# Optimization experiments

Measured on AMD Instinct MI355X. Metric: run time of the kernel, lower is better.

The kernel has to match this reference:

```python
import jax, jax.numpy as jnp
import numpy as np
from jax import lax

HEATMAP_THRESH = 0.1


def _conv(x, w, b, stride=1):
    y = lax.conv_general_dilated(x, w, (stride, stride), 'SAME',
                                 dimension_numbers=('NCHW', 'OIHW', 'NCHW'))
    return y + b[None, :, None, None]


def _maxpool2(x):
    return lax.reduce_window(x, -jnp.inf, lax.max, (1, 1, 2, 2), (1, 1, 2, 2), 'VALID')


def _up2(x):
    return jnp.repeat(jnp.repeat(x, 2, axis=2), 2, axis=3)


def _find_peaks_mask(hm, thresh):
    # Vectorized equivalent of the CPU nested-loop _find_peaks:
    # interior pixel is a peak iff v > thresh and v >= its 4 axial neighbors.
    c = hm[:, :, 1:-1, 1:-1]
    m = ((c > thresh)
         & (c >= hm[:, :, :-2, 1:-1]) & (c >= hm[:, :, 2:, 1:-1])
         & (c >= hm[:, :, 1:-1, :-2]) & (c >= hm[:, :, 1:-1, 2:]))
    return jnp.pad(m, ((0, 0), (0, 0), (1, 1), (1, 1)))  # border never a peak


def _param(key, shape):
    fan_in = int(np.prod(shape[1:]))
    return jax.random.normal(key, shape, jnp.float32) / np.sqrt(fan_in)


_SHAPES = {
    'w_d1': (32, 3, 3, 3), 'w_d2': (64, 32, 3, 3), 'w_bn': (128, 64, 3, 3),
    'w_u1': (64, 192, 3, 3), 'w_u2': (32, 96, 3, 3), 'w_seg': (1, 32, 1, 1),
    'w_p1': (64, 4, 3, 3), 'w_p2': (128, 64, 3, 3),
    'w_hm': (17, 128, 1, 1), 'w_paf': (32, 128, 1, 1),
}


def setup_inputs() -> dict:
    key = jax.random.key(0)
    ks = jax.random.split(key, 1 + len(_SHAPES))
    B, H, W = 8, 384, 384
    inp = {'x': jax.random.normal(ks[0], (B, 3, H, W), jnp.float32)}
    for i, (n, s) in enumerate(_SHAPES.items()):
        inp[n] = _param(ks[i + 1], s)
        inp[n.replace('w_', 'b_')] = jnp.zeros((s[0],), jnp.float32)
    return inp


def _forward(x, w_d1, b_d1, w_d2, b_d2, w_bn, b_bn, w_u1, b_u1, w_u2, b_u2,
             w_seg, b_seg, w_p1, b_p1, w_p2, b_p2, w_hm, b_hm, w_paf, b_paf):
    # --- UNet segmentation ---
    d1 = jax.nn.relu(_conv(x, w_d1, b_d1))                    # [B,32,384,384]
    d2 = jax.nn.relu(_conv(_maxpool2(d1), w_d2, b_d2))        # [B,64,192,192]
    bn = jax.nn.relu(_conv(_maxpool2(d2), w_bn, b_bn))        # [B,128,96,96]
    u1 = jax.nn.relu(_conv(jnp.concatenate([_up2(bn), d2], 1), w_u1, b_u1))  # [B,64,192,192]
    u2 = jax.nn.relu(_conv(jnp.concatenate([_up2(u1), d1], 1), w_u2, b_u2))  # [B,32,384,384]
    seg = _conv(u2, w_seg, b_seg)                             # [B,1,384,384]
    # --- Pose net on image + detached seg logits ---
    xp = jnp.concatenate([x, lax.stop_gradient(seg)], axis=1)  # detach()
    p1 = jax.nn.relu(_conv(xp, w_p1, b_p1, stride=2))          # [B,64,192,192]
    p2 = jax.nn.relu(_conv(p1, w_p2, b_p2, stride=2))          # [B,128,96,96]
    hm = _conv(p2, w_hm, b_hm)                                 # [B,17,96,96]
    paf = _conv(p2, w_paf, b_paf)                              # [B,32,96,96]
    return seg, hm, paf


def reference(x, w_d1, b_d1, w_d2, b_d2, w_bn, b_bn, w_u1, b_u1, w_u2, b_u2,
              w_seg, b_seg, w_p1, b_p1, w_p2, b_p2, w_hm, b_hm, w_paf, b_paf):
    seg, hm, paf = _forward(x, w_d1, b_d1, w_d2, b_d2, w_bn, b_bn, w_u1, b_u1,
                            w_u2, b_u2, w_seg, b_seg, w_p1, b_p1, w_p2, b_p2,
                            w_hm, b_hm, w_paf, b_paf)
    # jit-friendly replacement for the variable-length python peak lists:
    # boolean mask over [B,K,h,w]; (x,y) coords recoverable via jnp.nonzero offline.
    peaks = _find_peaks_mask(hm, HEATMAP_THRESH)
    return seg, hm, paf, peaks
```

## Files before the change

kernel.cpp:

```cpp
#include <hip/hip_runtime.h>


#define BS 256
#define BSW 512

typedef _Float16 half8 __attribute__((ext_vector_type(8)));
typedef float floatx4 __attribute__((ext_vector_type(4)));

#define LDSDW 20
#define PLT8 10000
#define ESTR 388

__global__ __launch_bounds__(BS) void packw_gen_kernel(
    const float* __restrict__ w, _Float16* __restrict__ bp, int Cin, int Cout)
{
    int total = (Cin >> 5) * 9 * (Cout >> 4) * 64;
    int tid = blockIdx.x * BS + threadIdx.x;
    if (tid >= total) return;
    int lane = tid & 63;
    int t = tid >> 6;
    int NTl = Cout >> 4;
    int nt = t % NTl; t /= NTl;
    int tap = t % 9;
    int chunk = t / 9;
    int q = lane >> 4, n = lane & 15;
    int co = nt * 16 + n;
    _Float16* ph = bp + (size_t)tid * 8;
    _Float16* pl = bp + (size_t)total * 8 + (size_t)tid * 8;
#pragma unroll
    for (int j = 0; j < 8; ++j) {
        int ci = chunk * 32 + q * 8 + j;
        float v = w[((size_t)co * Cin + ci) * 9 + tap];
        _Float16 h = (_Float16)v;
        ph[j] = h;
        pl[j] = (_Float16)(v - (float)h);
    }
}

__global__ __launch_bounds__(BS) void packw_1x1_kernel(
    const float* __restrict__ w, _Float16* __restrict__ bp, int Cin, int NTl, int Cout)
{
    int total = (Cin >> 5) * NTl * 64;
    int tid = blockIdx.x * BS + threadIdx.x;
    if (tid >= total) return;
    int lane = tid & 63;
    int t = tid >> 6;
    int nt = t % NTl;
    int chunk = t / NTl;
    int q = lane >> 4, n = lane & 15;
    int co = nt * 16 + n;
    _Float16* ph = bp + (size_t)tid * 8;
    _Float16* pl = bp + (size_t)total * 8 + (size_t)tid * 8;
#pragma unroll
    for (int j = 0; j < 8; ++j) {
        int ci = chunk * 32 + q * 8 + j;
        float v = (co < Cout) ? w[(size_t)co * Cin + ci] : 0.f;
        _Float16 h = (_Float16)v;
        ph[j] = h;
        pl[j] = (_Float16)(v - (float)h);
    }
}

template <int CHUNKS, int NT, int HH, int WW, int OUTMODE>
__global__ __launch_bounds__(BS) void conv3x3_mfma_kernel(
    const float* __restrict__ in_,
    const _Float16* __restrict__ bp,
    const float* __restrict__ bias,
    float* __restrict__ out,
    _Float16* __restrict__ osph,
    _Float16* __restrict__ ospl)
{
    constexpr int PL = 4 * 34 * LDSDW;
    constexpr int EPI = 64 * NT * 16;
    constexpr int LDS_DW = (2 * PL > EPI) ? 2 * PL : EPI;
    __shared__ unsigned int lds[LDS_DW];

    int xblks = WW / 32;
    int b = blockIdx.x;
    int xb = b % xblks; b /= xblks;
    int yp = b % (HH / 2);
    int n  = b / (HH / 2);
    int y0 = yp * 2;
    int x0 = xb * 32;

    int tid = threadIdx.x;
    int lane = tid & 63, wv = tid >> 6;
    int m = lane & 15, q = lane >> 4;
    int lrow = wv >> 1;
    int lx   = (wv & 1) * 16;

    floatx4 acc[NT];
#pragma unroll
    for (int nt = 0; nt < NT; ++nt) acc[nt] = (floatx4){0.f, 0.f, 0.f, 0.f};

    const int planeW = CHUNKS * 9 * NT * 64 * 8;

    for (int chunk = 0; chunk < CHUNKS; ++chunk) {
        __syncthreads();
        for (int e = tid; e < 4 * 34 * 4; e += BS) {
            int xi = e % 34;
            int rest = e / 34;
            int oct = rest & 3;
            int row = rest >> 2;
            int iy = y0 - 1 + row, gx = x0 - 1 + xi;
            bool ok = (iy >= 0 && iy < HH && gx >= 0 && gx < WW);
            const float* gp = in_ +
                ((size_t)(n * (CHUNKS * 32) + chunk * 32 + oct * 8) * HH + iy) * WW + gx;
            half8 hv, lv;
#pragma unroll
            for (int j = 0; j < 8; ++j) {
                float v = ok ? gp[(size_t)j * HH * WW] : 0.f;
                _Float16 h = (_Float16)v;
                hv[j] = h;
                lv[j] = (_Float16)(v - (float)h);
            }
            int base = (row * 34 + xi) * LDSDW + oct * 4;
            *(half8*)((char*)lds + (size_t)base * 4) = hv;
            *(half8*)((char*)lds + ((size_t)PL + base) * 4) = lv;
        }
        __syncthreads();
#pragma unroll
        for (int ky = 0; ky < 3; ++ky) {
#pragma unroll
            for (int kx = 0; kx < 3; ++kx) {
                int row = lrow + ky;
                int xi  = lx + m + kx;
                int adw = (row * 34 + xi) * LDSDW + q * 4;
                half8 ah = *(const half8*)((const char*)lds + (size_t)adw * 4);
                half8 al = *(const half8*)((const char*)lds + ((size_t)PL + adw) * 4);
                int tap = ky * 3 + kx;
                const _Float16* bpp = bp + ((size_t)(chunk * 9 + tap) * NT) * 64 * 8;
#pragma unroll
                for (int nt = 0; nt < NT; ++nt) {
                    half8 bh = *(const half8*)(bpp + ((size_t)nt * 64 + lane) * 8);
                    half8 bl = *(const half8*)(bpp + planeW + ((size_t)nt * 64 + lane) * 8);
                    acc[nt] = __builtin_amdgcn_mfma_f32_16x16x32_f16(ah, bh, acc[nt], 0, 0, 0);
                    acc[nt] = __builtin_amdgcn_mfma_f32_16x16x32_f16(ah, bl, acc[nt], 0, 0, 0);
                    acc[nt] = __builtin_amdgcn_mfma_f32_16x16x32_f16(al, bh, acc[nt], 0, 0, 0);
                }
            }
        }
    }

    __syncthreads();
#pragma unroll
    for (int nt = 0; nt < NT; ++nt) {
#pragma unroll
        for (int r = 0; r < 4; ++r) {
            int co = nt * 16 + m;
            int pxl = wv * 16 + q * 4 + r;
            ((float*)lds)[co * 64 + pxl] = acc[nt][r];
        }
    }
    __syncthreads();
    if (OUTMODE != 1) {
        constexpr int thPerCo = 256 / (NT * 16);
        constexpr int pxPerTh = 64 / thPerCo;
        int co = tid / thPerCo;
        int sub = tid % thPerCo;
        int pxb = sub * pxPerTh;
        float bb = bias[co];
#pragma unroll
        for (int u = 0; u < pxPerTh; u += 4) {
            int p = pxb + u;
            int row = y0 + (p >> 5), xx = x0 + (p & 31);
            const float* lp = (const float*)lds + co * 64 + p;
            float4 vv = *(const float4*)lp;
            vv.x = fmaxf(vv.x + bb, 0.f);
            vv.y = fmaxf(vv.y + bb, 0.f);
            vv.z = fmaxf(vv.z + bb, 0.f);
            vv.w = fmaxf(vv.w + bb, 0.f);
            *(float4*)(out + ((size_t)(n * NT * 16 + co) * HH + row) * WW + xx) = vv;
        }
    }
    if (OUTMODE >= 1) {
        constexpr int OCTS = NT * 2;
        for (int it = tid; it < OCTS * 64; it += BS) {
            int px = it & 63;
            int oct = it >> 6;
            int row = y0 + (px >> 5), xx = x0 + (px & 31);
            half8 hv, lv;
#pragma unroll
            for (int j = 0; j < 8; ++j) {
                float v = fmaxf(((float*)lds)[(oct * 8 + j) * 64 + px] + bias[oct * 8 + j], 0.f);
                _Float16 hh = (_Float16)v;
                hv[j] = hh;
                lv[j] = (_Float16)(v - (float)hh);
            }
            size_t oaddr = ((size_t)((n * OCTS + oct) * HH + row) * WW + xx) * 8;
            *(half8*)(osph + oaddr) = hv;
            *(half8*)(ospl + oaddr) = lv;
        }
    }
}

template <int CHUNKS, int NT, int WI>
__global__ __launch_bounds__(BS) void conv3x3s2_mfma_kernel(
    const float* __restrict__ in_,
    const _Float16* __restrict__ bp,
    const float* __restrict__ bias,
    float* __restrict__ out)
{
    constexpr int WO = WI / 2;
    constexpr int PLs = 5 * 68 * LDSDW;
    constexpr int EPI = 64 * NT * 16;
    constexpr int LDS_DW = (2 * PLs > EPI) ? 2 * PLs : EPI;
    __shared__ unsigned int lds[LDS_DW];

    int xblks = WO / 32;
    int b = blockIdx.x;
    int xb = b % xblks; b /= xblks;
    int yp = b % (WO / 2);
    int n  = b / (WO / 2);
    int y0 = yp * 2;
    int x0 = xb * 32;

    int tid = threadIdx.x;
    int lane = tid & 63, wv = tid >> 6;
    int m = lane & 15, q = lane >> 4;
    int lrow = wv >> 1;
    int lx   = (wv & 1) * 16;

    floatx4 acc[NT];
#pragma unroll
    for (int nt = 0; nt < NT; ++nt) acc[nt] = (floatx4){0.f, 0.f, 0.f, 0.f};

    const int planeW = CHUNKS * 9 * NT * 64 * 8;

    for (int chunk = 0; chunk < CHUNKS; ++chunk) {
        __syncthreads();
        for (int e = tid; e < 5 * 68 * 4; e += BS) {
            int xi = e % 68;
            int rest = e / 68;
            int oct = rest & 3;
            int row = rest >> 2;
            int iy = 2 * y0 + row, ix = 2 * x0 + xi;
            bool ok = (xi < 65 && iy < WI && ix < WI);
            const float* gp = in_ +
                ((size_t)(n * (CHUNKS * 32) + chunk * 32 + oct * 8) * WI + iy) * WI + ix;
            half8 hv, lv;
#pragma unroll
            for (int j = 0; j < 8; ++j) {
                float v = ok ? gp[(size_t)j * WI * WI] : 0.f;
                _Float16 h = (_Float16)v;
                hv[j] = h;
                lv[j] = (_Float16)(v - (float)h);
            }
            int pos = (xi & 1) * 34 + (xi >> 1);
            int base = (row * 68 + pos) * LDSDW + oct * 4;
            *(half8*)((char*)lds + (size_t)base * 4) = hv;
            *(half8*)((char*)lds + ((size_t)PLs + base) * 4) = lv;
        }
        __syncthreads();
#pragma unroll
        for (int ky = 0; ky < 3; ++ky) {
#pragma unroll
            for (int kx = 0; kx < 3; ++kx) {
                int row = 2 * lrow + ky;
                int pos = (kx & 1) * 34 + (lx + m) + (kx >> 1);
                int adw = (row * 68 + pos) * LDSDW + q * 4;
                half8 ah = *(const half8*)((const char*)lds + (size_t)adw * 4);
                half8 al = *(const half8*)((const char*)lds + ((size_t)PLs + adw) * 4);
                int tap = ky * 3 + kx;
                const _Float16* bpp = bp + ((size_t)(chunk * 9 + tap) * NT) * 64 * 8;
#pragma unroll
                for (int nt = 0; nt < NT; ++nt) {
                    half8 bh = *(const half8*)(bpp + ((size_t)nt * 64 + lane) * 8);
                    half8 bl = *(const half8*)(bpp + planeW + ((size_t)nt * 64 + lane) * 8);
                    acc[nt] = __builtin_amdgcn_mfma_f32_16x16x32_f16(ah, bh, acc[nt], 0, 0, 0);
                    acc[nt] = __builtin_amdgcn_mfma_f32_16x16x32_f16(ah, bl, acc[nt], 0, 0, 0);
                    acc[nt] = __builtin_amdgcn_mfma_f32_16x16x32_f16(al, bh, acc[nt], 0, 0, 0);
                }
            }
        }
    }

    __syncthreads();
#pragma unroll
    for (int nt = 0; nt < NT; ++nt) {
#pragma unroll
        for (int r = 0; r < 4; ++r) {
            int co = nt * 16 + m;
            int pxl = wv * 16 + q * 4 + r;
            ((float*)lds)[co * 64 + pxl] = acc[nt][r];
        }
    }
    __syncthreads();
    {
        constexpr int thPerCo = 256 / (NT * 16);
        constexpr int pxPerTh = 64 / thPerCo;
        int co = tid / thPerCo;
        int sub = tid % thPerCo;
        int pxb = sub * pxPerTh;
        float bb = bias[co];
#pragma unroll
        for (int u = 0; u < pxPerTh; u += 4) {
            int p = pxb + u;
            int row = y0 + (p >> 5), xx = x0 + (p & 31);
            const float* lp = (const float*)lds + co * 64 + p;
            float4 vv = *(const float4*)lp;
            vv.x = fmaxf(vv.x + bb, 0.f);
            vv.y = fmaxf(vv.y + bb, 0.f);
            vv.z = fmaxf(vv.z + bb, 0.f);
            vv.w = fmaxf(vv.w + bb, 0.f);
            *(float4*)(out + ((size_t)(n * NT * 16 + co) * WO + row) * WO + xx) = vv;
        }
    }
}

template <int CHUNKS, int NT>
__global__ __launch_bounds__(BS) void conv1x1_mfma_kernel(
    const float* __restrict__ in_,
    const _Float16* __restrict__ bp,
    const float* __restrict__ bias,
    float* __restrict__ out,
    int Cout, int HW)
{
    constexpr int PL1 = 64 * LDSDW;
    constexpr int EPI = 64 * NT * 16;
    constexpr int LDS_DW = (2 * PL1 > EPI) ? 2 * PL1 : EPI;
    __shared__ unsigned int lds[LDS_DW];

    int pblks = HW / 64;
    int b = blockIdx.x;
    int pb = b % pblks;
    int n  = b / pblks;
    int sp0 = pb * 64;

    int tid = threadIdx.x;
    int lane = tid & 63, wv = tid >> 6;
    int m = lane & 15, q = lane >> 4;

    floatx4 acc[NT];
#pragma unroll
    for (int nt = 0; nt < NT; ++nt) acc[nt] = (floatx4){0.f, 0.f, 0.f, 0.f};

    const int planeW = CHUNKS * NT * 64 * 8;

    for (int chunk = 0; chunk < CHUNKS; ++chunk) {
        __syncthreads();
        {
            int px = tid & 63;
            int oct = tid >> 6;
            const float* gp = in_ +
                ((size_t)(n * (CHUNKS * 32) + chunk * 32 + oct * 8)) * HW + sp0 + px;
            half8 hv, lv;
#pragma unroll
            for (int j = 0; j < 8; ++j) {
                float v = gp[(size_t)j * HW];
                _Float16 h = (_Float16)v;
                hv[j] = h;
                lv[j] = (_Float16)(v - (float)h);
            }
            int base = px * LDSDW + oct * 4;
            *(half8*)((char*)lds + (size_t)base * 4) = hv;
            *(half8*)((char*)lds + ((size_t)PL1 + base) * 4) = lv;
        }
        __syncthreads();
        {
            int adw = (wv * 16 + m) * LDSDW + q * 4;
            half8 ah = *(const half8*)((const char*)lds + (size_t)adw * 4);
            half8 al = *(const half8*)((const char*)lds + ((size_t)PL1 + adw) * 4);
            const _Float16* bpp = bp + ((size_t)chunk * NT) * 64 * 8;
#pragma unroll
            for (int nt = 0; nt < NT; ++nt) {
                half8 bh = *(const half8*)(bpp + ((size_t)nt * 64 + lane) * 8);
                half8 bl = *(const half8*)(bpp + planeW + ((size_t)nt * 64 + lane) * 8);
                acc[nt] = __builtin_amdgcn_mfma_f32_16x16x32_f16(ah, bh, acc[nt], 0, 0, 0);
                acc[nt] = __builtin_amdgcn_mfma_f32_16x16x32_f16(ah, bl, acc[nt], 0, 0, 0);
                acc[nt] = __builtin_amdgcn_mfma_f32_16x16x32_f16(al, bh, acc[nt], 0, 0, 0);
            }
        }
    }

    __syncthreads();
#pragma unroll
    for (int nt = 0; nt < NT; ++nt) {
#pragma unroll
        for (int r = 0; r < 4; ++r) {
            ((float*)lds)[(nt * 16 + m) * 64 + wv * 16 + q * 4 + r] = acc[nt][r];
        }
    }
    __syncthreads();
    {
        constexpr int thPerCo = 256 / (NT * 16);
        constexpr int pxPerTh = 64 / thPerCo;
        int co = tid / thPerCo;
        int g  = tid % thPerCo;
        if (co < Cout) {
            float bb = bias[co];
            const float* lp = (const float*)lds + co * 64 + g * pxPerTh;
            float* op = out + ((size_t)(n * Cout + co)) * HW + sp0 + g * pxPerTh;
#pragma unroll
            for (int u = 0; u < pxPerTh; u += 4) {
                float4 vv = *(const float4*)(lp + u);
                vv.x += bb; vv.y += bb; vv.z += bb; vv.w += bb;
                *(float4*)(op + u) = vv;
            }
        }
    }
}

__global__ __launch_bounds__(BSW) void u1_mfma_kernel(
    const _Float16* __restrict__ bnh, const _Float16* __restrict__ bnl,
    const _Float16* __restrict__ d2h, const _Float16* __restrict__ d2l,
    const _Float16* __restrict__ bp,
    const float* __restrict__ b_u1,
    _Float16* __restrict__ oh, _Float16* __restrict__ ol_)
{
    __shared__ unsigned int lds[2 * PLT8];
    const int Ho = 192, Wo = 192;
    int b = blockIdx.x;
    int xb = b % 4; b /= 4;
    int yb = b % 24;
    int n  = b / 24;
    int y0 = yb * 8;
    int x0 = xb * 48;

    int tid = threadIdx.x;
    int lane = tid & 63, wv = tid >> 6;
    int m = lane & 15, q = lane >> 4;
    int yr = y0 + wv;

    floatx4 acc[3][4];
#pragma unroll
    for (int mt = 0; mt < 3; ++mt)
#pragma unroll
        for (int nt = 0; nt < 4; ++nt) acc[mt][nt] = (floatx4){0.f, 0.f, 0.f, 0.f};

    const int hh0 = (y0 - 1) >> 1;
    const int hx0 = (x0 - 1) >> 1;

    for (int chunk = 0; chunk < 6; ++chunk) {
        __syncthreads();
        if (chunk < 4) {
            for (int e = tid; e < 6 * 26 * 4; e += BSW) {
                int xi = e % 26;
                int rest = e / 26;
                int oct = rest & 3;
                int row = rest >> 2;
                int hy = hh0 + row, hx = hx0 + xi;
                half8 hv = {}, lv = {};
                if (hy >= 0 && hy < 96 && hx >= 0 && hx < 96) {
                    size_t ga = ((size_t)((n * 16 + chunk * 4 + oct) * 96 + hy) * 96 + hx) * 8;
                    hv = *(const half8*)(bnh + ga);
                    lv = *(const half8*)(bnl + ga);
                }
                int base = (row * 50 + xi) * LDSDW + oct * 4;
                *(half8*)((char*)lds + (size_t)base * 4) = hv;
                *(half8*)((char*)lds + ((size_t)PLT8 + base) * 4) = lv;
            }
        } else {
            for (int e = tid; e < 10 * 50 * 4; e += BSW) {
                int xi = e % 50;
                int rest = e / 50;
                int oct = rest & 3;
                int row = rest >> 2;
                int iy = y0 - 1 + row, gx = x0 - 1 + xi;
                half8 hv = {}, lv = {};
                if (iy >= 0 && iy < Ho && gx >= 0 && gx < Wo) {
                    size_t ga = ((size_t)((n * 8 + (chunk - 4) * 4 + oct) * Ho + iy) * Wo + gx) * 8;
                    hv = *(const half8*)(d2h + ga);
                    lv = *(const half8*)(d2l + ga);
                }
                int base = (row * 50 + xi) * LDSDW + oct * 4;
                *(half8*)((char*)lds + (size_t)base * 4) = hv;
                *(half8*)((char*)lds + ((size_t)PLT8 + base) * 4) = lv;
            }
        }
        __syncthreads();
#pragma unroll
        for (int ky = 0; ky < 3; ++ky) {
#pragma unroll
            for (int kx = 0; kx < 3; ++kx) {
                int tap = ky * 3 + kx;
                const _Float16* bpp = bp + ((size_t)(chunk * 9 + tap) * 4) * 64 * 8;
                half8 bh[4], bl[4];
#pragma unroll
                for (int nt = 0; nt < 4; ++nt) {
                    bh[nt] = *(const half8*)(bpp + ((size_t)nt * 64 + lane) * 8);
                    bl[nt] = *(const half8*)(bpp + 110592 + ((size_t)nt * 64 + lane) * 8);
                }
                int row;
                if (chunk < 4) row = ((yr + ky - 1) >> 1) - hh0;
                else           row = wv + ky;
#pragma unroll
                for (int mt = 0; mt < 3; ++mt) {
                    int px = 16 * mt + m;
                    int xi = (chunk < 4) ? (((x0 + px + kx - 1) >> 1) - hx0)
                                         : (px + kx);
                    int adw = (row * 50 + xi) * LDSDW + q * 4;
                    half8 ah = *(const half8*)((const char*)lds + (size_t)adw * 4);
                    half8 al = *(const half8*)((const char*)lds + ((size_t)PLT8 + adw) * 4);
#pragma unroll
                    for (int nt = 0; nt < 4; ++nt) {
                        acc[mt][nt] = __builtin_amdgcn_mfma_f32_16x16x32_f16(ah, bh[nt], acc[mt][nt], 0, 0, 0);
                        acc[mt][nt] = __builtin_amdgcn_mfma_f32_16x16x32_f16(ah, bl[nt], acc[mt][nt], 0, 0, 0);
                        acc[mt][nt] = __builtin_amdgcn_mfma_f32_16x16x32_f16(al, bh[nt], acc[mt][nt], 0, 0, 0);
                    }
                }
            }
        }
    }

#pragma unroll
    for (int h = 0; h < 2; ++h) {
        __syncthreads();
#pragma unroll
        for (int ntl = 0; ntl < 2; ++ntl) {
#pragma unroll
            for (int mt = 0; mt < 3; ++mt) {
#pragma unroll
                for (int r = 0; r < 4; ++r) {
                    ((float*)lds)[(ntl * 16 + m) * ESTR + wv * 48 + 16 * mt + q * 4 + r]
                        = acc[mt][h * 2 + ntl][r];
                }
            }
        }
        __syncthreads();
        for (int it = tid; it < 4 * 384; it += BSW) {
            int px = it % 384;
            int ol = it / 384;
            int row = y0 + px / 48, xx = x0 + px % 48;
            half8 hv, lv;
#pragma unroll
            for (int j = 0; j < 8; ++j) {
                int col = ol * 8 + j;
                float v = fmaxf(((float*)lds)[col * ESTR + px] + b_u1[h * 32 + col], 0.f);
                _Float16 hh = (_Float16)v;
                hv[j] = hh;
                lv[j] = (_Float16)(v - (float)hh);
            }
            size_t oaddr = ((size_t)((n * 8 + h * 4 + ol) * Ho + row) * Wo + xx) * 8;
            *(half8*)(oh + oaddr) = hv;
            *(half8*)(ol_ + oaddr) = lv;
        }
    }
}

__global__ __launch_bounds__(BSW) void u2seg_mfma_kernel(
    const _Float16* __restrict__ u1h, const _Float16* __restrict__ u1l,
    const _Float16* __restrict__ d1h, const _Float16* __restrict__ d1l,
    const _Float16* __restrict__ bp,
    const float* __restrict__ b_u2,
    const float* __restrict__ w_seg,
    const float* __restrict__ b_seg,
    float* __restrict__ seg)
{
    __shared__ unsigned int lds[2 * PLT8];
    const int Ho = 384, Wo = 384;
    int b = blockIdx.x;
    int xb = b % 8; b /= 8;
    int yb = b % 48;
    int n  = b / 48;
    int y0 = yb * 8;
    int x0 = xb * 48;

    int tid = threadIdx.x;
    int lane = tid & 63, wv = tid >> 6;
    int m = lane & 15, q = lane >> 4;
    int yr = y0 + wv;

    floatx4 acc[3][2];
#pragma unroll
    for (int mt = 0; mt < 3; ++mt) {
        acc[mt][0] = (floatx4){0.f, 0.f, 0.f, 0.f};
        acc[mt][1] = (floatx4){0.f, 0.f, 0.f, 0.f};
    }

    const int hh0 = (y0 - 1) >> 1;
    const int hx0 = (x0 - 1) >> 1;

    for (int chunk = 0; chunk < 3; ++chunk) {
        __syncthreads();
        if (chunk < 2) {
            for (int e = tid; e < 6 * 26 * 4; e += BSW) {
                int xi = e % 26;
                int rest = e / 26;
                int oct = rest & 3;
                int row = rest >> 2;
                int hy = hh0 + row, hx = hx0 + xi;
                half8 hv = {}, lv = {};
                if (hy >= 0 && hy < 192 && hx >= 0 && hx < 192) {
                    size_t ga = ((size_t)((n * 8 + chunk * 4 + oct) * 192 + hy) * 192 + hx) * 8;
                    hv = *(const half8*)(u1h + ga);
                    lv = *(const half8*)(u1l + ga);
                }
                int base = (row * 50 + xi) * LDSDW + oct * 4;
                *(half8*)((char*)lds + (size_t)base * 4) = hv;
                *(half8*)((char*)lds + ((size_t)PLT8 + base) * 4) = lv;
            }
        } else {
            for (int e = tid; e < 10 * 50 * 4; e += BSW) {
                int xi = e % 50;
                int rest = e / 50;
                int oct = rest & 3;
                int row = rest >> 2;
                int iy = y0 - 1 + row, gx = x0 - 1 + xi;
                half8 hv = {}, lv = {};
                if (iy >= 0 && iy < Ho && gx >= 0 && gx < Wo) {
                    size_t ga = ((size_t)((n * 4 + oct) * Ho + iy) * Wo + gx) * 8;
                    hv = *(const half8*)(d1h + ga);
                    lv = *(const half8*)(d1l + ga);
                }
                int base = (row * 50 + xi) * LDSDW + oct * 4;
                *(half8*)((char*)lds + (size_t)base * 4) = hv;
                *(half8*)((char*)lds + ((size_t)PLT8 + base) * 4) = lv;
            }
        }
        __syncthreads();
#pragma unroll
        for (int ky = 0; ky < 3; ++ky) {
#pragma unroll
            for (int kx = 0; kx < 3; ++kx) {
                int tap = ky * 3 + kx;
                const _Float16* bpp = bp + ((size_t)(chunk * 9 + tap) * 2) * 64 * 8;
                half8 bh0 = *(const half8*)(bpp + (size_t)lane * 8);
                half8 bl0 = *(const half8*)(bpp + 27648 + (size_t)lane * 8);
                half8 bh1 = *(const half8*)(bpp + ((size_t)64 + lane) * 8);
                half8 bl1 = *(const half8*)(bpp + 27648 + ((size_t)64 + lane) * 8);
                int row;
                if (chunk < 2) row = ((yr + ky - 1) >> 1) - hh0;
                else           row = wv + ky;
#pragma unroll
                for (int mt = 0; mt < 3; ++mt) {
                    int px = 16 * mt + m;
                    int xi = (chunk < 2) ? (((x0 + px + kx - 1) >> 1) - hx0)
                                         : (px + kx);
                    int adw = (row * 50 + xi) * LDSDW + q * 4;
                    half8 ah = *(const half8*)((const char*)lds + (size_t)adw * 4);
                    half8 al = *(const half8*)((const char*)lds + ((size_t)PLT8 + adw) * 4);
                    acc[mt][0] = __builtin_amdgcn_mfma_f32_16x16x32_f16(ah, bh0, acc[mt][0], 0, 0, 0);
                    acc[mt][0] = __builtin_amdgcn_mfma_f32_16x16x32_f16(ah, bl0, acc[mt][0], 0, 0, 0);
                    acc[mt][0] = __builtin_amdgcn_mfma_f32_16x16x32_f16(al, bh0, acc[mt][0], 0, 0, 0);
                    acc[mt][1] = __builtin_amdgcn_mfma_f32_16x16x32_f16(ah, bh1, acc[mt][1], 0, 0, 0);
                    acc[mt][1] = __builtin_amdgcn_mfma_f32_16x16x32_f16(ah, bl1, acc[mt][1], 0, 0, 0);
                    acc[mt][1] = __builtin_amdgcn_mfma_f32_16x16x32_f16(al, bh1, acc[mt][1], 0, 0, 0);
                }
            }
        }
    }

    float bb0 = b_u2[m], bb1 = b_u2[16 + m];
    float ws0 = w_seg[m], ws1 = w_seg[16 + m];
    float bseg = b_seg[0];
#pragma unroll
    for (int mt = 0; mt < 3; ++mt) {
        float sr[4];
#pragma unroll
        for (int r = 0; r < 4; ++r) {
            float p = ws0 * fmaxf(acc[mt][0][r] + bb0, 0.f)
                    + ws1 * fmaxf(acc[mt][1][r] + bb1, 0.f);
            p += __shfl_xor(p, 1);
            p += __shfl_xor(p, 2);
            p += __shfl_xor(p, 4);
            p += __shfl_xor(p, 8);
            sr[r] = p + bseg;
        }
        if (m == 0) {
            float4 o; o.x = sr[0]; o.y = sr[1]; o.z = sr[2]; o.w = sr[3];
            *(float4*)(seg + ((size_t)n * Ho + yr) * Wo + x0 + 16 * mt + q * 4) = o;
        }
    }
}


template <int UPA, int TCO, int SPLIT>
__global__ __launch_bounds__(BS, 2) void conv3x3_x8_kernel(
    const float* __restrict__ inA, int Ca,
    const float* __restrict__ inB, int Cb,
    const float* __restrict__ w, const float* __restrict__ b,
    float* __restrict__ out,
    int N, int H, int W, int Cout, int do_relu,
    _Float16* __restrict__ osph, _Float16* __restrict__ ospl)
{
    const int W8 = W >> 3;
    int idx = blockIdx.x * BS + threadIdx.x;
    int total = N * H * W8;
    if (idx >= total) return;
    int x8 = idx % W8;
    int t  = idx / W8;
    int y  = t % H;
    int n  = t / H;
    int x0 = x8 << 3;
    const int co0 = blockIdx.y * TCO;
    const bool left_ok  = (x0 > 0);
    const bool right_ok = (x0 + 8 < W);
    const int Cin = Ca + Cb;

    float acc[TCO][8];
#pragma unroll
    for (int j = 0; j < TCO; ++j) {
        float bv = b[co0 + j];
#pragma unroll
        for (int p = 0; p < 8; ++p) acc[j][p] = bv;
    }

    for (int ci = 0; ci < Cin; ++ci) {
        float v[3][10];
#pragma unroll
        for (int ky = 0; ky < 3; ++ky) {
            int iy = y + ky - 1;
            if (iy < 0 || iy >= H) {
#pragma unroll
                for (int p = 0; p < 10; ++p) v[ky][p] = 0.f;
                continue;
            }
            if (UPA == 2 && ci < Ca) {
                const float* r = inA + ((size_t)(n * Ca + ci) * (H >> 1) + (iy >> 1)) * (W >> 1);
                int xh = x0 >> 1;
                float sm = left_ok  ? r[xh - 1] : 0.f;
                float4 qq = *(const float4*)(r + xh);
                float s4 = right_ok ? r[xh + 4] : 0.f;
                v[ky][0] = sm;
                v[ky][1] = qq.x; v[ky][2] = qq.x;
                v[ky][3] = qq.y; v[ky][4] = qq.y;
                v[ky][5] = qq.z; v[ky][6] = qq.z;
                v[ky][7] = qq.w; v[ky][8] = qq.w;
                v[ky][9] = s4;
            } else {
                const float* r = (ci < Ca)
                    ? inA + ((size_t)(n * Ca + ci) * H + iy) * W
                    : inB + ((size_t)(n * Cb + (ci - Ca)) * H + iy) * W;
                v[ky][0] = left_ok ? r[x0 - 1] : 0.f;
                float4 q0 = *(const float4*)(r + x0);
                float4 q1 = *(const float4*)(r + x0 + 4);
                v[ky][1] = q0.x; v[ky][2] = q0.y; v[ky][3] = q0.z; v[ky][4] = q0.w;
                v[ky][5] = q1.x; v[ky][6] = q1.y; v[ky][7] = q1.z; v[ky][8] = q1.w;
                v[ky][9] = right_ok ? r[x0 + 8] : 0.f;
            }
        }
#pragma unroll
        for (int j = 0; j < TCO; ++j) {
            const float* wp = w + ((size_t)(co0 + j) * Cin + ci) * 9;
#pragma unroll
            for (int ky = 0; ky < 3; ++ky) {
                float w0 = wp[ky * 3 + 0], w1 = wp[ky * 3 + 1], w2 = wp[ky * 3 + 2];
#pragma unroll
                for (int p = 0; p < 8; ++p)
                    acc[j][p] += w0 * v[ky][p] + w1 * v[ky][p + 1] + w2 * v[ky][p + 2];
            }
        }
    }

    if (SPLIT) {
#pragma unroll
        for (int p = 0; p < 8; ++p) {
            half8 hv, lv;
#pragma unroll
            for (int j = 0; j < 8; ++j) {
                float v = acc[j][p];
                if (do_relu) v = fmaxf(v, 0.f);
                _Float16 hh = (_Float16)v;
                hv[j] = hh;
                lv[j] = (_Float16)(v - (float)hh);
            }
            size_t oaddr = ((size_t)((n * (Cout >> 3) + (co0 >> 3)) * H + y) * W + x0 + p) * 8;
            *(half8*)(osph + oaddr) = hv;
            *(half8*)(ospl + oaddr) = lv;
        }
    } else {
#pragma unroll
        for (int j = 0; j < TCO; ++j) {
#pragma unroll
            for (int p = 0; p < 8; ++p)
                if (do_relu) acc[j][p] = fmaxf(acc[j][p], 0.f);
            float* o = out + ((size_t)(n * Cout + co0 + j) * H + y) * W + x0;
            float4 q0; q0.x = acc[j][0]; q0.y = acc[j][1]; q0.z = acc[j][2]; q0.w = acc[j][3];
            float4 q1; q1.x = acc[j][4]; q1.y = acc[j][5]; q1.z = acc[j][6]; q1.w = acc[j][7];
            *(float4*)o = q0;
            *(float4*)(o + 4) = q1;
        }
    }
}

template <int TCO>
__global__ __launch_bounds__(BS) void conv3x3_s2_co_kernel(
    const float* __restrict__ inA, int Ca,
    const float* __restrict__ inB, int Cb,
    const float* __restrict__ w, const float* __restrict__ b,
    float* __restrict__ out,
    int N, int Hi, int Wi, int Cout, int do_relu)
{
    const int Ho = Hi >> 1, Wo = Wi >> 1, Woq = Wo >> 2;
    int idx = blockIdx.x * BS + threadIdx.x;
    int total = N * Ho * Woq;
    if (idx >= total) return;
    int q  = idx % Woq;
    int t  = idx / Woq;
    int oy = t % Ho;
    int n  = t / Ho;
    int ox0 = q << 2;
    int ix0 = ox0 << 1;
    const int co0 = blockIdx.y * TCO;
    const bool right_ok = (ix0 + 8 < Wi);
    const int Cin = Ca + Cb;

    float acc[TCO][4];
#pragma unroll
    for (int j = 0; j < TCO; ++j) {
        float bv = b[co0 + j];
        acc[j][0] = bv; acc[j][1] = bv; acc[j][2] = bv; acc[j][3] = bv;
    }

    for (int ci = 0; ci < Cin; ++ci) {
        const float* base = (ci < Ca)
            ? inA + (size_t)(n * Ca + ci) * Hi * Wi
            : inB + (size_t)(n * Cb + (ci - Ca)) * Hi * Wi;
        float v[3][9];
#pragma unroll
        for (int ky = 0; ky < 3; ++ky) {
            int iy = 2 * oy + ky;
            if (iy >= Hi) {
#pragma unroll
                for (int p = 0; p < 9; ++p) v[ky][p] = 0.f;
                continue;
            }
            const float* r = base + (size_t)iy * Wi + ix0;
            float4 a = *(const float4*)r;
            float4 c = *(const float4*)(r + 4);
            v[ky][0] = a.x; v[ky][1] = a.y; v[ky][2] = a.z; v[ky][3] = a.w;
            v[ky][4] = c.x; v[ky][5] = c.y; v[ky][6] = c.z; v[ky][7] = c.w;
            v[ky][8] = right_ok ? r[8] : 0.f;
        }
#pragma unroll
        for (int j = 0; j < TCO; ++j) {
            const float* wp = w + ((size_t)(co0 + j) * Cin + ci) * 9;
#pragma unroll
            for (int ky = 0; ky < 3; ++ky) {
                float w0 = wp[ky * 3 + 0], w1 = wp[ky * 3 + 1], w2 = wp[ky * 3 + 2];
#pragma unroll
                for (int p = 0; p < 4; ++p)
                    acc[j][p] += w0 * v[ky][2 * p] + w1 * v[ky][2 * p + 1] + w2 * v[ky][2 * p + 2];
            }
        }
    }

#pragma unroll
    for (int j = 0; j < TCO; ++j) {
        float4 o;
        o.x = acc[j][0]; o.y = acc[j][1]; o.z = acc[j][2]; o.w = acc[j][3];
        if (do_relu) {
            o.x = fmaxf(o.x, 0.f); o.y = fmaxf(o.y, 0.f);
            o.z = fmaxf(o.z, 0.f); o.w = fmaxf(o.w, 0.f);
        }
        *(float4*)(out + ((size_t)(n * Cout + co0 + j) * Ho + oy) * Wo + ox0) = o;
    }
}

__global__ __launch_bounds__(BS) void maxpool2_kernel(
    const float* __restrict__ in, float* __restrict__ out, int NC, int H, int W)
{
    int Ho = H >> 1, Wo = W >> 1, Woq = Wo >> 2;
    int idx = blockIdx.x * BS + threadIdx.x;
    int total = NC * Ho * Woq;
    if (idx >= total) return;
    int x4 = idx % Woq;
    int t  = idx / Woq;
    int y  = t % Ho;
    int c  = t / Ho;
    const float* r0 = in + ((size_t)c * H + 2 * y) * W + 8 * x4;
    const float* r1 = r0 + W;
    float4 a0 = *(const float4*)r0;
    float4 a1 = *(const float4*)(r0 + 4);
    float4 b0 = *(const float4*)r1;
    float4 b1 = *(const float4*)(r1 + 4);
    float4 o;
    o.x = fmaxf(fmaxf(a0.x, a0.y), fmaxf(b0.x, b0.y));
    o.y = fmaxf(fmaxf(a0.z, a0.w), fmaxf(b0.z, b0.w));
    o.z = fmaxf(fmaxf(a1.x, a1.y), fmaxf(b1.x, b1.y));
    o.w = fmaxf(fmaxf(a1.z, a1.w), fmaxf(b1.z, b1.w));
    *(float4*)(out + ((size_t)c * Ho + y) * Wo + 4 * x4) = o;
}

__global__ __launch_bounds__(BS) void peaks_kernel(
    const float* __restrict__ hm, float* __restrict__ out,
    int NC, int H, int W, float thresh)
{
    int idx = blockIdx.x * BS + threadIdx.x;
    int total = NC * H * W;
    if (idx >= total) return;
    int x = idx % W;
    int t = idx / W;
    int y = t % H;
    int c = t / H;
    float r = 0.f;
    if (x >= 1 && x < W - 1 && y >= 1 && y < H - 1) {
        const float* base = hm + (size_t)c * H * W;
        float cv = base[y * W + x];
        if (cv > thresh &&
            cv >= base[(y - 1) * W + x] &&
            cv >= base[(y + 1) * W + x] &&
            cv >= base[y * W + (x - 1)] &&
            cv >= base[y * W + (x + 1)])
            r = 1.f;
    }
    out[idx] = r;
}

static inline int nblk(long n) { return (int)((n + BS - 1) / BS); }

extern "C" void kernel_launch(void* const* d_in, const int* in_sizes, int n_in,
                              void* d_out, int out_size, void* d_ws, size_t ws_size,
                              hipStream_t stream)
{
    const float* x     = (const float*)d_in[0];
    const float* w_d1  = (const float*)d_in[1];  const float* b_d1  = (const float*)d_in[2];
    const float* w_d2  = (const float*)d_in[3];  const float* b_d2  = (const float*)d_in[4];
    const float* w_bn  = (const float*)d_in[5];  const float* b_bn  = (const float*)d_in[6];
    const float* w_u1  = (const float*)d_in[7];  const float* b_u1  = (const float*)d_in[8];
    const float* w_u2  = (const float*)d_in[9];  const float* b_u2  = (const float*)d_in[10];
    const float* w_seg = (const float*)d_in[11]; const float* b_seg = (const float*)d_in[12];
    const float* w_p1  = (const float*)d_in[13]; const float* b_p1  = (const float*)d_in[14];
    const float* w_p2  = (const float*)d_in[15]; const float* b_p2  = (const float*)d_in[16];
    const float* w_hm  = (const float*)d_in[17]; const float* b_hm  = (const float*)d_in[18];
    const float* w_paf = (const float*)d_in[19]; const float* b_paf = (const float*)d_in[20];

    const int N = 8, H = 384, W = 384;
    const int H2 = 192, W2 = 192, H4 = 96, W4 = 96;

    float* ws = (float*)d_ws;
    float* d1   = ws + 18874368;
    float* pd1  = ws;
    float* d2f  = ws + 9437184;
    _Float16* d2sp_h = (_Float16*)(ws + 28311552);
    _Float16* d2sp_l = (_Float16*)(ws + 37748736);
    float* pd2  = ws + 47185920;
    _Float16* bnsp_h = (_Float16*)(ws + 18874368);
    _Float16* bnsp_l = (_Float16*)(ws + 23592960);
    _Float16* u1sp_h = (_Float16*)(ws);
    _Float16* u1sp_l = (_Float16*)(ws + 9437184);
    _Float16* d1sp_h = (_Float16*)(ws + 18874368);
    _Float16* d1sp_l = (_Float16*)(ws + 37748736);
    float* p1   = ws;
    float* p2   = ws + 18874368;

    float* out_seg   = (float*)d_out;
    float* out_hm    = out_seg + 1179648;
    float* out_paf   = out_hm + 1253376;
    float* out_peaks = out_paf + 2359296;
    _Float16* bp_u1  = (_Float16*)(out_seg + 4792320);
    _Float16* bp_u2  = (_Float16*)(out_seg + 4902912);
    _Float16* bp_d2  = (_Float16*)(out_seg + 4930560);
    _Float16* bp_bn  = (_Float16*)(out_seg + 4948992);
    _Float16* bp_p2  = (_Float16*)(out_seg + 5022720);
    _Float16* bp_hm  = (_Float16*)(out_seg + 5096448);
    _Float16* bp_paf = (_Float16*)(out_seg + 5100544);

    packw_gen_kernel<<<nblk(13824), BS, 0, stream>>>(w_u1, bp_u1, 192, 64);
    packw_gen_kernel<<<nblk(3456),  BS, 0, stream>>>(w_u2, bp_u2, 96, 32);
    packw_gen_kernel<<<nblk(2304),  BS, 0, stream>>>(w_d2, bp_d2, 32, 64);
    packw_gen_kernel<<<nblk(9216),  BS, 0, stream>>>(w_bn, bp_bn, 64, 128);
    packw_gen_kernel<<<nblk(9216),  BS, 0, stream>>>(w_p2, bp_p2, 64, 128);
    packw_1x1_kernel<<<nblk(512),   BS, 0, stream>>>(w_hm, bp_hm, 128, 2, 17);
    packw_1x1_kernel<<<nblk(512),   BS, 0, stream>>>(w_paf, bp_paf, 128, 2, 32);
    {
        dim3 g(nblk((long)N * H * (W / 8)), 32 / 8);
        conv3x3_x8_kernel<1, 8, 0><<<g, BS, 0, stream>>>(
            x, 3, nullptr, 0, w_d1, b_d1, d1, N, H, W, 32, 1, nullptr, nullptr);
    }
    maxpool2_kernel<<<nblk((long)N * 32 * H2 * (W2 / 4)), BS, 0, stream>>>(d1, pd1, N * 32, H, W);
    conv3x3_mfma_kernel<1, 4, 192, 192, 2><<<8 * 96 * 6, BS, 0, stream>>>(
        pd1, bp_d2, b_d2, d2f, d2sp_h, d2sp_l);
    maxpool2_kernel<<<nblk((long)N * 64 * H4 * (W4 / 4)), BS, 0, stream>>>(d2f, pd2, N * 64, H2, W2);
    conv3x3_mfma_kernel<2, 8, 96, 96, 1><<<8 * 48 * 3, BS, 0, stream>>>(
        pd2, bp_bn, b_bn, nullptr, bnsp_h, bnsp_l);
    u1_mfma_kernel<<<8 * 24 * 4, BSW, 0, stream>>>(
        bnsp_h, bnsp_l, d2sp_h, d2sp_l, bp_u1, b_u1, u1sp_h, u1sp_l);
    {
        dim3 g(nblk((long)N * H * (W / 8)), 32 / 8);
        conv3x3_x8_kernel<1, 8, 1><<<g, BS, 0, stream>>>(
            x, 3, nullptr, 0, w_d1, b_d1, nullptr, N, H, W, 32, 1, d1sp_h, d1sp_l);
    }
    u2seg_mfma_kernel<<<8 * 48 * 8, BSW, 0, stream>>>(
        u1sp_h, u1sp_l, d1sp_h, d1sp_l, bp_u2, b_u2, w_seg, b_seg, out_seg);
    {
        dim3 g(nblk((long)N * H2 * (W2 / 4)), 64 / 8);
        conv3x3_s2_co_kernel<8><<<g, BS, 0, stream>>>(
            x, 3, out_seg, 1, w_p1, b_p1, p1, N, H, W, 64, 1);
    }
    conv3x3s2_mfma_kernel<2, 8, 192><<<8 * 48 * 3, BS, 0, stream>>>(
        p1, bp_p2, b_p2, p2);
    conv1x1_mfma_kernel<4, 2><<<8 * 144, BS, 0, stream>>>(
        p2, bp_hm, b_hm, out_hm, 17, H4 * W4);
    conv1x1_mfma_kernel<4, 2><<<8 * 144, BS, 0, stream>>>(
        p2, bp_paf, b_paf, out_paf, 32, H4 * W4);
    peaks_kernel<<<nblk((long)N * 17 * H4 * W4), BS, 0, stream>>>(
        out_hm, out_peaks, N * 17, H4, W4, 0.1f);
}
```

Measured before the change: 965.0 us.

## Produce channel-octet split fp16 hi/lo activations upstream for all MFMA conv inputs

The producers (maxpool, the stride-2 p1 conv and the p2 conv epilogue) now write activations pre-split into fp16 high and low parts in a channel-octet-interleaved layout. The MFMA conv kernels then load them with vectorized half8 reads instead of eight strided fp32 loads plus per-element conversion. This removes redundant conversion work, since halo tiles get reconverted across blocks, and makes the global loads coalesced. In exchange, producer epilogues do more work and the intermediate buffers change size and aliasing.

Measured after the change: 962.9 us. Within noise of the previous version (-0.2%).

```diff
diff --git a/kernel.cpp b/kernel.cpp
--- a/kernel.cpp
+++ b/kernel.cpp
@@ -61,9 +61,53 @@
     }
 }
 
+__global__ __launch_bounds__(BS) void maxpool2_split_kernel(
+    const float* __restrict__ in, _Float16* __restrict__ oh, _Float16* __restrict__ ol,
+    int N, int Coct, int H, int W)
+{
+    int Ho = H >> 1, Wo = W >> 1, Woq = Wo >> 2;
+    int idx = blockIdx.x * BS + threadIdx.x;
+    int total = N * Coct * Ho * Woq;
+    if (idx >= total) return;
+    int x4 = idx % Woq;
+    int t  = idx / Woq;
+    int y  = t % Ho; t /= Ho;
+    int oct = t % Coct;
+    int n  = t / Coct;
+    int C = Coct * 8;
+    float m[8][4];
+#pragma unroll
+    for (int j = 0; j < 8; ++j) {
+        const float* r0 = in + ((size_t)((n * C + oct * 8 + j) * H + 2 * y)) * W + 8 * x4;
+        const float* r1 = r0 + W;
+        float4 a0 = *(const float4*)r0;
+        float4 a1 = *(const float4*)(r0 + 4);
+        float4 b0 = *(const float4*)r1;
+        float4 b1 = *(const float4*)(r1 + 4);
+        m[j][0] = fmaxf(fmaxf(a0.x, a0.y), fmaxf(b0.x, b0.y));
+        m[j][1] = fmaxf(fmaxf(a0.z, a0.w), fmaxf(b0.z, b0.w));
+        m[j][2] = fmaxf(fmaxf(a1.x, a1.y), fmaxf(b1.x, b1.y));
+        m[j][3] = fmaxf(fmaxf(a1.z, a1.w), fmaxf(b1.z, b1.w));
+    }
+#pragma unroll
+    for (int p = 0; p < 4; ++p) {
+        half8 hv, lv;
+#pragma unroll
+        for (int j = 0; j < 8; ++j) {
+            float v = m[j][p];
+            _Float16 h = (_Float16)v;
+            hv[j] = h;
+            lv[j] = (_Float16)(v - (float)h);
+        }
+        size_t oa = ((size_t)((n * Coct + oct) * Ho + y) * Wo + 4 * x4 + p) * 8;
+        *(half8*)(oh + oa) = hv;
+        *(half8*)(ol + oa) = lv;
+    }
+}
+
 template <int CHUNKS, int NT, int HH, int WW, int OUTMODE>
-__global__ __launch_bounds__(BS) void conv3x3_mfma_kernel(
-    const float* __restrict__ in_,
+__global__ __launch_bounds__(BS) void conv3x3s_mfma_kernel(
+    const _Float16* __restrict__ inh, const _Float16* __restrict__ inl,
     const _Float16* __restrict__ bp,
     const float* __restrict__ bias,
     float* __restrict__ out,
@@ -103,16 +147,11 @@
             int oct = rest & 3;
             int row = rest >> 2;
             int iy = y0 - 1 + row, gx = x0 - 1 + xi;
-            bool ok = (iy >= 0 && iy < HH && gx >= 0 && gx < WW);
-            const float* gp = in_ +
-                ((size_t)(n * (CHUNKS * 32) + chunk * 32 + oct * 8) * HH + iy) * WW + gx;
-            half8 hv, lv;
-#pragma unroll
-            for (int j = 0; j < 8; ++j) {
-                float v = ok ? gp[(size_t)j * HH * WW] : 0.f;
-                _Float16 h = (_Float16)v;
-                hv[j] = h;
-                lv[j] = (_Float16)(v - (float)h);
+            half8 hv = {}, lv = {};
+            if (iy >= 0 && iy < HH && gx >= 0 && gx < WW) {
+                size_t ga = ((size_t)((n * (CHUNKS * 4) + chunk * 4 + oct) * HH + iy) * WW + gx) * 8;
+                hv = *(const half8*)(inh + ga);
+                lv = *(const half8*)(inl + ga);
             }
             int base = (row * 34 + xi) * LDSDW + oct * 4;
             *(half8*)((char*)lds + (size_t)base * 4) = hv;
@@ -195,11 +234,11 @@
 }
 
 template <int CHUNKS, int NT, int WI>
-__global__ __launch_bounds__(BS) void conv3x3s2_mfma_kernel(
-    const float* __restrict__ in_,
+__global__ __launch_bounds__(BS) void conv3x3s2s_mfma_kernel(
+    const _Float16* __restrict__ inh, const _Float16* __restrict__ inl,
     const _Float16* __restrict__ bp,
     const float* __restrict__ bias,
-    float* __restrict__ out)
+    _Float16* __restrict__ oh, _Float16* __restrict__ ol_)
 {
     constexpr int WO = WI / 2;
     constexpr int PLs = 5 * 68 * LDSDW;
@@ -235,16 +274,11 @@
             int oct = rest & 3;
             int row = rest >> 2;
             int iy = 2 * y0 + row, ix = 2 * x0 + xi;
-            bool ok = (xi < 65 && iy < WI && ix < WI);
-            const float* gp = in_ +
-                ((size_t)(n * (CHUNKS * 32) + chunk * 32 + oct * 8) * WI + iy) * WI + ix;
-            half8 hv, lv;
-#pragma unroll
-            for (int j = 0; j < 8; ++j) {
-                float v = ok ? gp[(size_t)j * WI * WI] : 0.f;
-                _Float16 h = (_Float16)v;
-                hv[j] = h;
-                lv[j] = (_Float16)(v - (float)h);
+            half8 hv = {}, lv = {};
+            if (xi < 65 && iy < WI && ix < WI) {
+                size_t ga = ((size_t)((n * (CHUNKS * 4) + chunk * 4 + oct) * WI + iy) * WI + ix) * 8;
+                hv = *(const half8*)(inh + ga);
+                lv = *(const half8*)(inl + ga);
             }
             int pos = (xi & 1) * 34 + (xi >> 1);
             int base = (row * 68 + pos) * LDSDW + oct * 4;
@@ -287,30 +321,29 @@
     }
     __syncthreads();
     {
-        constexpr int thPerCo = 256 / (NT * 16);
-        constexpr int pxPerTh = 64 / thPerCo;
-        int co = tid / thPerCo;
-        int sub = tid % thPerCo;
-        int pxb = sub * pxPerTh;
-        float bb = bias[co];
-#pragma unroll
-        for (int u = 0; u < pxPerTh; u += 4) {
-            int p = pxb + u;
-            int row = y0 + (p >> 5), xx = x0 + (p & 31);
-            const float* lp = (const float*)lds + co * 64 + p;
-            float4 vv = *(const float4*)lp;
-            vv.x = fmaxf(vv.x + bb, 0.f);
-            vv.y = fmaxf(vv.y + bb, 0.f);
-            vv.z = fmaxf(vv.z + bb, 0.f);
-            vv.w = fmaxf(vv.w + bb, 0.f);
-            *(float4*)(out + ((size_t)(n * NT * 16 + co) * WO + row) * WO + xx) = vv;
+        constexpr int OCTS = NT * 2;
+        for (int it = tid; it < OCTS * 64; it += BS) {
+            int px = it & 63;
+            int oct = it >> 6;
+            int row = y0 + (px >> 5), xx = x0 + (px & 31);
+            half8 hv, lv;
+#pragma unroll
+            for (int j = 0; j < 8; ++j) {
+                float v = fmaxf(((float*)lds)[(oct * 8 + j) * 64 + px] + bias[oct * 8 + j], 0.f);
+                _Float16 hh = (_Float16)v;
+                hv[j] = hh;
+                lv[j] = (_Float16)(v - (float)hh);
+            }
+            size_t oaddr = ((size_t)((n * OCTS + oct) * WO + row) * WO + xx) * 8;
+            *(half8*)(oh + oaddr) = hv;
+            *(half8*)(ol_ + oaddr) = lv;
         }
     }
 }
 
 template <int CHUNKS, int NT>
-__global__ __launch_bounds__(BS) void conv1x1_mfma_kernel(
-    const float* __restrict__ in_,
+__global__ __launch_bounds__(BS) void conv1x1s_mfma_kernel(
+    const _Float16* __restrict__ inh, const _Float16* __restrict__ inl,
     const _Float16* __restrict__ bp,
     const float* __restrict__ bias,
     float* __restrict__ out,
@@ -342,16 +375,9 @@
         {
             int px = tid & 63;
             int oct = tid >> 6;
-            const float* gp = in_ +
-                ((size_t)(n * (CHUNKS * 32) + chunk * 32 + oct * 8)) * HW + sp0 + px;
-            half8 hv, lv;
-#pragma unroll
-            for (int j = 0; j < 8; ++j) {
-                float v = gp[(size_t)j * HW];
-                _Float16 h = (_Float16)v;
-                hv[j] = h;
-                lv[j] = (_Float16)(v - (float)h);
-            }
+            size_t ga = (((size_t)(n * (CHUNKS * 4) + chunk * 4 + oct)) * HW + sp0 + px) * 8;
+            half8 hv = *(const half8*)(inh + ga);
+            half8 lv = *(const half8*)(inl + ga);
             int base = px * LDSDW + oct * 4;
             *(half8*)((char*)lds + (size_t)base * 4) = hv;
             *(half8*)((char*)lds + ((size_t)PL1 + base) * 4) = lv;
@@ -774,13 +800,14 @@
     }
 }
 
-template <int TCO>
+template <int TCO, int SPLIT>
 __global__ __launch_bounds__(BS) void conv3x3_s2_co_kernel(
     const float* __restrict__ inA, int Ca,
     const float* __restrict__ inB, int Cb,
     const float* __restrict__ w, const float* __restrict__ b,
     float* __restrict__ out,
-    int N, int Hi, int Wi, int Cout, int do_relu)
+    int N, int Hi, int Wi, int Cout, int do_relu,
+    _Float16* __restrict__ osph, _Float16* __restrict__ ospl)
 {
     const int Ho = Hi >> 1, Wo = Wi >> 1, Woq = Wo >> 2;
     int idx = blockIdx.x * BS + threadIdx.x;
@@ -836,41 +863,34 @@
         }
     }
 
-#pragma unroll
-    for (int j = 0; j < TCO; ++j) {
-        float4 o;
-        o.x = acc[j][0]; o.y = acc[j][1]; o.z = acc[j][2]; o.w = acc[j][3];
-        if (do_relu) {
-            o.x = fmaxf(o.x, 0.f); o.y = fmaxf(o.y, 0.f);
-            o.z = fmaxf(o.z, 0.f); o.w = fmaxf(o.w, 0.f);
-        }
-        *(float4*)(out + ((size_t)(n * Cout + co0 + j) * Ho + oy) * Wo + ox0) = o;
-    }
-}
-
-__global__ __launch_bounds__(BS) void maxpool2_kernel(
-    const float* __restrict__ in, float* __restrict__ out, int NC, int H, int W)
-{
-    int Ho = H >> 1, Wo = W >> 1, Woq = Wo >> 2;
-    int idx = blockIdx.x * BS + threadIdx.x;
-    int total = NC * Ho * Woq;
-    if (idx >= total) return;
-    int x4 = idx % Woq;
-    int t  = idx / Woq;
-    int y  = t % Ho;
-    int c  = t / Ho;
-    const float* r0 = in + ((size_t)c * H + 2 * y) * W + 8 * x4;
-    const float* r1 = r0 + W;
-    float4 a0 = *(const float4*)r0;
-    float4 a1 = *(const float4*)(r0 + 4);
-    float4 b0 = *(const float4*)r1;
-    float4 b1 = *(const float4*)(r1 + 4);
-    float4 o;
-    o.x = fmaxf(fmaxf(a0.x, a0.y), fmaxf(b0.x, b0.y));
-    o.y = fmaxf(fmaxf(a0.z, a0.w), fmaxf(b0.z, b0.w));
-    o.z = fmaxf(fmaxf(a1.x, a1.y), fmaxf(b1.x, b1.y));
-    o.w = fmaxf(fmaxf(a1.z, a1.w), fmaxf(b1.z, b1.w));
-    *(float4*)(out + ((size_t)c * Ho + y) * Wo + 4 * x4) = o;
+    if (SPLIT) {
+#pragma unroll
+        for (int p = 0; p < 4; ++p) {
+            half8 hv, lv;
+#pragma unroll
+            for (int j = 0; j < 8; ++j) {
+                float v = acc[j][p];
+                if (do_relu) v = fmaxf(v, 0.f);
+                _Float16 hh = (_Float16)v;
+                hv[j] = hh;
+                lv[j] = (_Float16)(v - (float)hh);
+            }
+            size_t oaddr = ((size_t)((n * (Cout >> 3) + (co0 >> 3)) * Ho + oy) * Wo + ox0 + p) * 8;
+            *(half8*)(osph + oaddr) = hv;
+            *(half8*)(ospl + oaddr) = lv;
+        }
+    } else {
+#pragma unroll
+        for (int j = 0; j < TCO; ++j) {
+            float4 o;
+            o.x = acc[j][0]; o.y = acc[j][1]; o.z = acc[j][2]; o.w = acc[j][3];
+            if (do_relu) {
+                o.x = fmaxf(o.x, 0.f); o.y = fmaxf(o.y, 0.f);
+                o.z = fmaxf(o.z, 0.f); o.w = fmaxf(o.w, 0.f);
+            }
+            *(float4*)(out + ((size_t)(n * Cout + co0 + j) * Ho + oy) * Wo + ox0) = o;
+        }
+    }
 }
 
 __global__ __launch_bounds__(BS) void peaks_kernel(
@@ -921,19 +941,23 @@
 
     float* ws = (float*)d_ws;
     float* d1   = ws + 18874368;
-    float* pd1  = ws;
+    _Float16* pd1sp_h = (_Float16*)(ws);
+    _Float16* pd1sp_l = (_Float16*)(ws + 4718592);
     float* d2f  = ws + 9437184;
     _Float16* d2sp_h = (_Float16*)(ws + 28311552);
     _Float16* d2sp_l = (_Float16*)(ws + 37748736);
-    float* pd2  = ws + 47185920;
+    _Float16* pd2sp_h = (_Float16*)(ws + 47185920);
+    _Float16* pd2sp_l = (_Float16*)(ws + 49545216);
     _Float16* bnsp_h = (_Float16*)(ws + 18874368);
     _Float16* bnsp_l = (_Float16*)(ws + 23592960);
     _Float16* u1sp_h = (_Float16*)(ws);
     _Float16* u1sp_l = (_Float16*)(ws + 9437184);
     _Float16* d1sp_h = (_Float16*)(ws + 18874368);
     _Float16* d1sp_l = (_Float16*)(ws + 37748736);
-    float* p1   = ws;
-    float* p2   = ws + 18874368;
+    _Float16* p1sp_h = (_Float16*)(ws);
+    _Float16* p1sp_l = (_Float16*)(ws + 9437184);
+    _Float16* p2sp_h = (_Float16*)(ws + 18874368);
+    _Float16* p2sp_l = (_Float16*)(ws + 23592960);
 
     float* out_seg   = (float*)d_out;
     float* out_hm    = out_seg + 1179648;
@@ -959,12 +983,14 @@
         conv3x3_x8_kernel<1, 8, 0><<<g, BS, 0, stream>>>(
             x, 3, nullptr, 0, w_d1, b_d1, d1, N, H, W, 32, 1, nullptr, nullptr);
     }
-    maxpool2_kernel<<<nblk((long)N * 32 * H2 * (W2 / 4)), BS, 0, stream>>>(d1, pd1, N * 32, H, W);
-    conv3x3_mfma_kernel<1, 4, 192, 192, 2><<<8 * 96 * 6, BS, 0, stream>>>(
-        pd1, bp_d2, b_d2, d2f, d2sp_h, d2sp_l);
-    maxpool2_kernel<<<nblk((long)N * 64 * H4 * (W4 / 4)), BS, 0, stream>>>(d2f, pd2, N * 64, H2, W2);
-    conv3x3_mfma_kernel<2, 8, 96, 96, 1><<<8 * 48 * 3, BS, 0, stream>>>(
-        pd2, bp_bn, b_bn, nullptr, bnsp_h, bnsp_l);
+    maxpool2_split_kernel<<<nblk((long)8 * 4 * 192 * 48), BS, 0, stream>>>(
+        d1, pd1sp_h, pd1sp_l, N, 4, H, W);
+    conv3x3s_mfma_kernel<1, 4, 192, 192, 2><<<8 * 96 * 6, BS, 0, stream>>>(
+        pd1sp_h, pd1sp_l, bp_d2, b_d2, d2f, d2sp_h, d2sp_l);
+    maxpool2_split_kernel<<<nblk((long)8 * 8 * 96 * 24), BS, 0, stream>>>(
+        d2f, pd2sp_h, pd2sp_l, N, 8, H2, W2);
+    conv3x3s_mfma_kernel<2, 8, 96, 96, 1><<<8 * 48 * 3, BS, 0, stream>>>(
+        pd2sp_h, pd2sp_l, bp_bn, b_bn, nullptr, bnsp_h, bnsp_l);
     u1_mfma_kernel<<<8 * 24 * 4, BSW, 0, stream>>>(
         bnsp_h, bnsp_l, d2sp_h, d2sp_l, bp_u1, b_u1, u1sp_h, u1sp_l);
     {
@@ -976,15 +1002,15 @@
         u1sp_h, u1sp_l, d1sp_h, d1sp_l, bp_u2, b_u2, w_seg, b_seg, out_seg);
     {
         dim3 g(nblk((long)N * H2 * (W2 / 4)), 64 / 8);
-        conv3x3_s2_co_kernel<8><<<g, BS, 0, stream>>>(
-            x, 3, out_seg, 1, w_p1, b_p1, p1, N, H, W, 64, 1);
-    }
-    conv3x3s2_mfma_kernel<2, 8, 192><<<8 * 48 * 3, BS, 0, stream>>>(
-        p1, bp_p2, b_p2, p2);
-    conv1x1_mfma_kernel<4, 2><<<8 * 144, BS, 0, stream>>>(
-        p2, bp_hm, b_hm, out_hm, 17, H4 * W4);
-    conv1x1_mfma_kernel<4, 2><<<8 * 144, BS, 0, stream>>>(
-        p2, bp_paf, b_paf, out_paf, 32, H4 * W4);
+        conv3x3_s2_co_kernel<8, 1><<<g, BS, 0, stream>>>(
+            x, 3, out_seg, 1, w_p1, b_p1, nullptr, N, H, W, 64, 1, p1sp_h, p1sp_l);
+    }
+    conv3x3s2s_mfma_kernel<2, 8, 192><<<8 * 48 * 3, BS, 0, stream>>>(
+        p1sp_h, p1sp_l, bp_p2, b_p2, p2sp_h, p2sp_l);
+    conv1x1s_mfma_kernel<4, 2><<<8 * 144, BS, 0, stream>>>(
+        p2sp_h, p2sp_l, bp_hm, b_hm, out_hm, 17, H4 * W4);
+    conv1x1s_mfma_kernel<4, 2><<<8 * 144, BS, 0, stream>>>(
+        p2sp_h, p2sp_l, bp_paf, b_paf, out_paf, 32, H4 * W4);
     peaks_kernel<<<nblk((long)N * 17 * H4 * W4), BS, 0, stream>>>(
         out_hm, out_peaks, N * 17, H4, W4, 0.1f);
 }
```
